# Kernel optimization log

Hardware: AMD Instinct MI355X
Metric: run time of the kernel (lower is better)

## Reference

```python
import jax, jax.numpy as jnp
import numpy as np

N, LP, LD, D, H, GS = 16, 2048, 512, 256, 8, 4
HD = D // H           # head_size = 32
TAU = 1.0             # softmax_tau
ITERS = 4             # sinkhorn_iters
INF = 1.0e6


def setup_inputs() -> dict:
    key = jax.random.key(0)
    ks = jax.random.split(key, 10)
    inp = {
        "protein": jax.random.normal(ks[0], (N, LP, D), jnp.float32),
        "drug": jax.random.normal(ks[1], (N, LD, D), jnp.float32),
        "mask_prot": jax.random.bernoulli(ks[2], 0.9, (N, LP)),
        "mask_drug": jax.random.bernoulli(ks[3], 0.9, (N, LD)),
    }
    names = ["Wq_p", "Wk_p", "Wv_p", "Wq_d", "Wk_d", "Wv_d"]
    for i, name in enumerate(names):
        inp[name] = jax.random.normal(ks[4 + i], (D, D), jnp.float32) * (1.0 / np.sqrt(D))
    return inp


def _group(x, mask):
    n, L, d = x.shape
    g = L // GS
    xg = x.reshape(n, g, GS, d).mean(2)          # [N,G,D]
    mg = mask.reshape(n, g, GS).any(2)           # [N,G]
    return xg, mg


def _alpha_logits(logits, mask_row, mask_col):
    # logits: [N,L1,L2,H]; sinkhorn normalization as in the torch module
    n, L1, L2, h = logits.shape
    logits = logits * (1.0 / np.sqrt(HD))
    pair = mask_row[:, :, None, None] & mask_col[:, None, :, None]  # [N,L1,L2,1]
    logits = jnp.where(pair, logits, logits - INF)
    A = jax.nn.softmax((logits / TAU).reshape(n, L1 * L2, h), axis=1).reshape(n, L1, L2, h)
    valid = pair.astype(A.dtype)
    A = A * valid + 1e-12 * valid
    for _ in range(ITERS):
        row_sum = (A * valid).sum(2, keepdims=True) + 1e-12
        A = A / row_sum * valid
        col_sum = (A * valid).sum(1, keepdims=True) + 1e-12
        A = A / col_sum * valid
    return A * valid


def _proj(x, W):
    n, g, d = x.shape
    return (x @ W.T).reshape(n, g, H, HD)


def reference(protein, drug, mask_prot, mask_drug, Wq_p, Wk_p, Wv_p, Wq_d, Wk_d, Wv_d):
    pg, mp = _group(protein, mask_prot)   # [N,Gp,D], [N,Gp]
    dg, md = _group(drug, mask_drug)      # [N,Gd,D], [N,Gd]

    qp, kp, vp = _proj(pg, Wq_p), _proj(pg, Wk_p), _proj(pg, Wv_p)
    qd, kd, vd = _proj(dg, Wq_d), _proj(dg, Wk_d), _proj(dg, Wv_d)

    att = lambda q, k: jnp.einsum('blhd,bkhd->blkh', q, k)
    a_pp = _alpha_logits(att(qp, kp), mp, mp)
    a_pd = _alpha_logits(att(qp, kd), mp, md)
    a_dp = _alpha_logits(att(qd, kp), md, mp)
    a_dd = _alpha_logits(att(qd, kd), md, md)

    mix = lambda a, v: jnp.einsum('blkh,bkhd->blhd', a, v).reshape(a.shape[0], a.shape[1], D)
    prot_embedding = (mix(a_pp, vp) + mix(a_pd, vd)) * 0.5  # [N,Gp,D]
    drug_embedding = (mix(a_dp, vp) + mix(a_dd, vd)) * 0.5  # [N,Gd,D]

    # agg_mode == 'mean': masked mean over valid groups
    mpf = mp[..., None].astype(prot_embedding.dtype)
    mdf = md[..., None].astype(drug_embedding.dtype)
    prot_embed = (prot_embedding * mpf).sum(1) / mpf.sum(1)
    drug_embed = (drug_embedding * mdf).sum(1) / mdf.sum(1)

    query_embed = jnp.concatenate([prot_embed, drug_embed], axis=1)  # [N,2D]
    return query_embed, a_dp
```

## Files before the change

kernel.cpp:

```cpp
#include <hip/hip_runtime.h>
#include <hip/hip_bf16.h>

#define NB   16
#define DT   256
#define HT   8
#define HDT  32
#define GP   512
#define GD   128

using bf16x8 = __attribute__((ext_vector_type(8))) short;
using f32x4  = __attribute__((ext_vector_type(4))) float;

__device__ __forceinline__ short f2bf(float f) {
  __hip_bfloat16 h = __float2bfloat16(f);
  short s; __builtin_memcpy(&s, &h, 2);
  return s;
}

extern "C" __global__ void k_prep(const float* __restrict__ Wk,
                                  const float* __restrict__ Wq,
                                  short* __restrict__ Wk_bf, short* __restrict__ Wq_bf,
                                  float* __restrict__ sp, float* __restrict__ sd,
                                  int* __restrict__ cnt) {
  int gid = blockIdx.x * 256 + threadIdx.x;
  if (gid < 65536) Wk_bf[gid] = f2bf(Wk[gid]);
  else             Wq_bf[gid - 65536] = f2bf(Wq[gid - 65536]);
  if (gid < 4096) sp[gid] = 0.f;
  else if (gid < 8192) sd[gid - 4096] = 0.f;
  if (gid < 32) cnt[gid] = 0;
}

extern "C" __global__ __launch_bounds__(256)
void k_group(const float* __restrict__ protein, const float* __restrict__ drug,
             const int* __restrict__ mprot, const int* __restrict__ mdrug,
             short* __restrict__ pg_bf, short* __restrict__ dg_bf,
             int* __restrict__ mp_g, int* __restrict__ md_g,
             float* __restrict__ sp, float* __restrict__ sd,
             int* __restrict__ cnt) {
  int b = blockIdx.x;
  int t = threadIdx.x;
  int n, c0, G;
  const float* src; const int* msk; short* dst; float* ssum; int* mg; int* cdst;
  if (b < 256) { n = b >> 4; c0 = (b & 15) * 32; G = GP;
                 src = protein; msk = mprot; dst = pg_bf; ssum = sp; mg = mp_g;
                 cdst = cnt + n; }
  else { int bb = b - 256; n = bb >> 2; c0 = (bb & 3) * 32; G = GD;
         src = drug; msk = mdrug; dst = dg_bf; ssum = sd; mg = md_g;
         cdst = cnt + 16 + n; }

  __shared__ int gmask[32];
  if (t < 32) {
    const int* m = msk + ((size_t)n * G + c0 + t) * 4;
    int v = (m[0] | m[1] | m[2] | m[3]) ? 1 : 0;
    gmask[t] = v;
    mg[n * G + c0 + t] = v;
  }
  __syncthreads();
  if (t == 0) {
    int c = 0;
    #pragma unroll
    for (int i = 0; i < 32; ++i) c += gmask[i];
    atomicAdd(cdst, c);
  }

  float acc_s = 0.f;
  const float* bp = src + ((size_t)n * G + c0) * 1024 + t;
  #pragma unroll 4
  for (int gi = 0; gi < 32; ++gi) {
    const float* rp = bp + (size_t)gi * 1024;
    float gm = 0.25f * (rp[0] + rp[256] + rp[512] + rp[768]);
    dst[((size_t)n * G + c0 + gi) * 256 + t] = f2bf(gm);
    if (gmask[gi]) acc_s += gm;
  }
  atomicAdd(&ssum[n * 256 + t], acc_s);
}

extern "C" __global__ __launch_bounds__(256)
void k_projbf(const short* __restrict__ pg_bf, const short* __restrict__ dg_bf,
              const short* __restrict__ Wk_bf, const short* __restrict__ Wq_bf,
              short* __restrict__ kp_bf, short* __restrict__ qd_bf) {
  int b = blockIdx.x;
  int w = threadIdx.x >> 6, lane = threadIdx.x & 63;
  int c15 = lane & 15, g = lane >> 4;
  const short *A, *W; short* out; int rt;
  if (b < 128) { A = pg_bf; W = Wk_bf; out = kp_bf; rt = b * 4 + w; }
  else         { A = dg_bf; W = Wq_bf; out = qd_bf; rt = (b - 128) * 4 + w; }

  const short* ap = A + ((size_t)rt * 16 + c15) * 256;
  f32x4 acc[16];
  #pragma unroll
  for (int i = 0; i < 16; ++i) acc[i] = (f32x4){0.f, 0.f, 0.f, 0.f};

  #pragma unroll
  for (int ks = 0; ks < 8; ++ks) {
    bf16x8 af = *(const bf16x8*)(ap + ks * 32 + g * 8);
    #pragma unroll
    for (int ct = 0; ct < 16; ++ct) {
      bf16x8 bfr = *(const bf16x8*)(W + ((size_t)(ct * 16 + c15)) * 256 + ks * 32 + g * 8);
      acc[ct] = __builtin_amdgcn_mfma_f32_16x16x32_bf16(af, bfr, acc[ct], 0, 0, 0);
    }
  }
  #pragma unroll
  for (int ct = 0; ct < 16; ++ct) {
    #pragma unroll
    for (int r = 0; r < 4; ++r) {
      out[((size_t)rt * 16 + 4 * g + r) * 256 + ct * 16 + c15] = f2bf(acc[ct][r]);
    }
  }
}

extern "C" __global__ __launch_bounds__(256)
void k_embed(const float* __restrict__ sp, const float* __restrict__ sd,
             const float* __restrict__ Wvp, const float* __restrict__ Wvd,
             const int* __restrict__ cnt, float* __restrict__ out) {
  int n = blockIdx.x >> 3;
  int dchunk = (blockIdx.x & 7) * 32;
  int t = threadIdx.x;
  __shared__ float sps[256], sds[256];
  sps[t] = sp[n * 256 + t];
  sds[t] = sd[n * 256 + t];
  __syncthreads();
  int dloc = t >> 3, ks = (t & 7) * 32;
  int d = dchunk + dloc;
  const float* wp = Wvp + (size_t)d * 256 + ks;
  const float* wd = Wvd + (size_t)d * 256 + ks;
  float acc = 0.f;
  #pragma unroll
  for (int k = 0; k < 32; k += 4) {
    float4 a = *(const float4*)(wp + k);
    float4 c = *(const float4*)(wd + k);
    acc += sps[ks + k] * a.x + sps[ks + k + 1] * a.y + sps[ks + k + 2] * a.z + sps[ks + k + 3] * a.w
         + sds[ks + k] * c.x + sds[ks + k + 1] * c.y + sds[ks + k + 2] * c.z + sds[ks + k + 3] * c.w;
  }
  #pragma unroll
  for (int m = 1; m <= 4; m <<= 1) acc += __shfl_xor(acc, m, 64);
  if ((t & 7) == 0) {
    acc *= 0.5f;
    out[n * 512 + d]       = acc / (float)cnt[n];
    out[n * 512 + 256 + d] = acc / (float)cnt[16 + n];
  }
}

extern "C" __global__ __launch_bounds__(512, 2)
void k_scalars(const short* __restrict__ qd, const short* __restrict__ kp,
               const int* __restrict__ md_g, const int* __restrict__ mp_g,
               float* __restrict__ rcz) {
  int bid = blockIdx.x;
  int n = ((bid & 7) << 1) | ((bid >> 3) & 1);
  int h = bid >> 4;
  int tid = threadIdx.x;
  int w = tid >> 6, lane = tid & 63;
  int c15 = lane & 15, g = lane >> 4;

  __shared__ float c_s[GP];
  __shared__ float r_s[GD];
  __shared__ float t_s[GD];
  __shared__ float red[8][GP];
  __shared__ float z_sh, sr_sh, sc_sh, kv_sh;
  __shared__ int mp_sh[GP];
  __shared__ int md_sh[GD];

  if (tid < GP) { int m = mp_g[n * GP + tid]; mp_sh[tid] = m; c_s[tid] = m ? 1.f : 0.f; }
  if (tid < GD) { int m = md_g[n * GD + tid]; md_sh[tid] = m; r_s[tid] = m ? 1.f : 0.f; }
  if (tid == 0) z_sh = 0.f;
  __syncthreads();

  if (w == 0) {
    float v = (float)(mp_sh[lane] + mp_sh[lane + 64] + mp_sh[lane + 128] + mp_sh[lane + 192] +
                      mp_sh[lane + 256] + mp_sh[lane + 320] + mp_sh[lane + 384] + mp_sh[lane + 448]);
    #pragma unroll
    for (int m = 1; m <= 32; m <<= 1) v += __shfl_xor(v, m, 64);
    if (lane == 0) kv_sh = v;
  }

  int qrow = 16 * w + c15;
  bf16x8 af = *(const bf16x8*)(qd + ((size_t)(n * GD + qrow)) * 256 + h * HDT + g * 8);

  float p[32][4];
  #pragma unroll
  for (int ct = 0; ct < 32; ++ct) {
    int krow = 16 * ct + c15;
    bf16x8 bfr = *(const bf16x8*)(kp + ((size_t)(n * GP + krow)) * 256 + h * HDT + g * 8);
    f32x4 acc = __builtin_amdgcn_mfma_f32_16x16x32_bf16(af, bfr, (f32x4){0.f,0.f,0.f,0.f}, 0, 0, 0);
    int mcol = mp_sh[16 * ct + c15];
    #pragma unroll
    for (int r = 0; r < 4; ++r) {
      int row = 16 * w + 4 * g + r;
      p[ct][r] = (mcol && md_sh[row]) ? __expf(acc[r] * 0.17677669529663687f) : 0.f;
    }
  }

  {
    float pa0 = 0.f, pa1 = 0.f, pa2 = 0.f, pa3 = 0.f;
    #pragma unroll
    for (int ct = 0; ct < 32; ++ct) {
      pa0 += p[ct][0]; pa1 += p[ct][1]; pa2 += p[ct][2]; pa3 += p[ct][3];
    }
    #pragma unroll
    for (int m = 1; m <= 8; m <<= 1) {
      pa0 += __shfl_xor(pa0, m, 64); pa1 += __shfl_xor(pa1, m, 64);
      pa2 += __shfl_xor(pa2, m, 64); pa3 += __shfl_xor(pa3, m, 64);
    }
    if (c15 == 0) t_s[16 * w + 4 * g + 0] = pa0;
    if (c15 == 1) t_s[16 * w + 4 * g + 1] = pa1;
    if (c15 == 2) t_s[16 * w + 4 * g + 2] = pa2;
    if (c15 == 3) t_s[16 * w + 4 * g + 3] = pa3;
  }
  __syncthreads();
  if (tid < GD) atomicAdd(&z_sh, t_s[tid]);
  __syncthreads();
  float Zinv = 1.0f / z_sh;
  float Sc = kv_sh;

  #pragma unroll 1
  for (int it = 0; it < 4; ++it) {
    if (tid < GD) {
      float ti = t_s[tid] * Zinv + 1e-12f * Sc;
      float ri = r_s[tid];
      r_s[tid] = md_sh[tid] ? (ri / (ri * ti + 1e-12f)) : 0.f;
    }
    __syncthreads();
    if (w == 0) {
      float v = r_s[lane] + r_s[lane + 64];
      #pragma unroll
      for (int m = 1; m <= 32; m <<= 1) v += __shfl_xor(v, m, 64);
      if (lane == 0) sr_sh = v;
    }
    __syncthreads();
    float Sr = sr_sh;
    float rr0 = r_s[16 * w + 4 * g + 0];
    float rr1 = r_s[16 * w + 4 * g + 1];
    float rr2 = r_s[16 * w + 4 * g + 2];
    float rr3 = r_s[16 * w + 4 * g + 3];
    #pragma unroll
    for (int ct = 0; ct < 32; ++ct) {
      float u = p[ct][0] * rr0 + p[ct][1] * rr1 + p[ct][2] * rr2 + p[ct][3] * rr3;
      u += __shfl_xor(u, 16, 64);
      u += __shfl_xor(u, 32, 64);
      if (g == 0) red[w][16 * ct + c15] = u;
    }
    __syncthreads();
    {
      float cs = red[0][tid] + red[1][tid] + red[2][tid] + red[3][tid] +
                 red[4][tid] + red[5][tid] + red[6][tid] + red[7][tid];
      float uj = cs * Zinv + 1e-12f * Sr;
      float cj = c_s[tid];
      c_s[tid] = mp_sh[tid] ? (cj / (cj * uj + 1e-12f)) : 0.f;
    }
    __syncthreads();
    if (w == 0) {
      float v = c_s[lane] + c_s[lane + 64] + c_s[lane + 128] + c_s[lane + 192] +
                c_s[lane + 256] + c_s[lane + 320] + c_s[lane + 384] + c_s[lane + 448];
      #pragma unroll
      for (int m = 1; m <= 32; m <<= 1) v += __shfl_xor(v, m, 64);
      if (lane == 0) sc_sh = v;
    }
    __syncthreads();
    Sc = sc_sh;
    if (it < 3) {
      float pa0 = 0.f, pa1 = 0.f, pa2 = 0.f, pa3 = 0.f;
      #pragma unroll
      for (int ct = 0; ct < 32; ++ct) {
        float cv = c_s[16 * ct + c15];
        pa0 += p[ct][0] * cv; pa1 += p[ct][1] * cv;
        pa2 += p[ct][2] * cv; pa3 += p[ct][3] * cv;
      }
      #pragma unroll
      for (int m = 1; m <= 8; m <<= 1) {
        pa0 += __shfl_xor(pa0, m, 64); pa1 += __shfl_xor(pa1, m, 64);
        pa2 += __shfl_xor(pa2, m, 64); pa3 += __shfl_xor(pa3, m, 64);
      }
      if (c15 == 0) t_s[16 * w + 4 * g + 0] = pa0;
      if (c15 == 1) t_s[16 * w + 4 * g + 1] = pa1;
      if (c15 == 2) t_s[16 * w + 4 * g + 2] = pa2;
      if (c15 == 3) t_s[16 * w + 4 * g + 3] = pa3;
      __syncthreads();
    }
  }

  size_t rb = (size_t)(n * 8 + h) * 1024;
  if (tid < GD) rcz[rb + tid] = r_s[tid];
  if (tid < GP) rcz[rb + 128 + tid] = c_s[tid];
  if (tid == 0) rcz[rb + 640] = Zinv;
}

extern "C" __global__ __launch_bounds__(256)
void k_write(const short* __restrict__ qd, const short* __restrict__ kp,
             const float* __restrict__ rcz, float* __restrict__ out) {
  int bid = blockIdx.x;
  int n = ((bid & 7) << 1) | ((bid >> 3) & 1);
  int rest = bid >> 4;
  int rt = rest >> 2;
  int cc = rest & 3;
  int w = threadIdx.x >> 6, lane = threadIdx.x & 63;
  int c15 = lane & 15, g = lane >> 4;

  const short* qbase = qd + ((size_t)(n * GD + rt * 16 + c15)) * 256;
  bf16x8 af[8];
  #pragma unroll
  for (int h = 0; h < 8; ++h) af[h] = *(const bf16x8*)(qbase + h * HDT + g * 8);

  size_t rb = (size_t)n * 8 * 1024;
  float rv[8][4], zin[8];
  #pragma unroll
  for (int h = 0; h < 8; ++h) {
    const float* rp = rcz + rb + (size_t)h * 1024;
    #pragma unroll
    for (int r = 0; r < 4; ++r) rv[h][r] = rp[rt * 16 + 4 * g + r];
    zin[h] = rp[640];
  }

  #pragma unroll
  for (int ct = 0; ct < 2; ++ct) {
    int col = cc * 128 + w * 32 + ct * 16 + c15;
    f32x4 acc[8]; float cw[8];
    #pragma unroll
    for (int h = 0; h < 8; ++h) {
      bf16x8 bfr = *(const bf16x8*)(kp + ((size_t)(n * GP + col)) * 256 + h * HDT + g * 8);
      acc[h] = __builtin_amdgcn_mfma_f32_16x16x32_bf16(af[h], bfr, (f32x4){0.f,0.f,0.f,0.f}, 0, 0, 0);
      cw[h] = rcz[rb + (size_t)h * 1024 + 128 + col];
    }
    #pragma unroll
    for (int r = 0; r < 4; ++r) {
      int row = rt * 16 + 4 * g + r;
      float4 lo, hi;
      lo.x = rv[0][r] * (__expf(acc[0][r] * 0.17677669529663687f) * zin[0] + 1e-12f) * cw[0];
      lo.y = rv[1][r] * (__expf(acc[1][r] * 0.17677669529663687f) * zin[1] + 1e-12f) * cw[1];
      lo.z = rv[2][r] * (__expf(acc[2][r] * 0.17677669529663687f) * zin[2] + 1e-12f) * cw[2];
      lo.w = rv[3][r] * (__expf(acc[3][r] * 0.17677669529663687f) * zin[3] + 1e-12f) * cw[3];
      hi.x = rv[4][r] * (__expf(acc[4][r] * 0.17677669529663687f) * zin[4] + 1e-12f) * cw[4];
      hi.y = rv[5][r] * (__expf(acc[5][r] * 0.17677669529663687f) * zin[5] + 1e-12f) * cw[5];
      hi.z = rv[6][r] * (__expf(acc[6][r] * 0.17677669529663687f) * zin[6] + 1e-12f) * cw[6];
      hi.w = rv[7][r] * (__expf(acc[7][r] * 0.17677669529663687f) * zin[7] + 1e-12f) * cw[7];
      float* dst = out + 8192 + (((size_t)(n * GD + row)) * GP + col) * 8;
      *(float4*)dst = lo;
      *(float4*)(dst + 4) = hi;
    }
  }
}

extern "C" void kernel_launch(void* const* d_in, const int* in_sizes, int n_in,
                              void* d_out, int out_size, void* d_ws, size_t ws_size,
                              hipStream_t stream) {
  const float* protein = (const float*)d_in[0];
  const float* drug    = (const float*)d_in[1];
  const int*   mprot   = (const int*)d_in[2];
  const int*   mdrug   = (const int*)d_in[3];
  const float* Wk_p = (const float*)d_in[5];
  const float* Wv_p = (const float*)d_in[6];
  const float* Wq_d = (const float*)d_in[7];
  const float* Wv_d = (const float*)d_in[9];
  float* out = (float*)d_out;

  char* wsb = (char*)d_ws;
  short* pg_bf = (short*)wsb;                 wsb += (size_t)NB * GP * 256 * 2;
  short* dg_bf = (short*)wsb;                 wsb += (size_t)NB * GD * 256 * 2;
  short* kp_bf = (short*)wsb;                 wsb += (size_t)NB * GP * 256 * 2;
  short* qd_bf = (short*)wsb;                 wsb += (size_t)NB * GD * 256 * 2;
  short* Wk_bf = (short*)wsb;                 wsb += 65536 * 2;
  short* Wq_bf = (short*)wsb;                 wsb += 65536 * 2;
  float* sp    = (float*)wsb;                 wsb += 4096 * 4;
  float* sd    = (float*)wsb;                 wsb += 4096 * 4;
  float* rcz   = (float*)wsb;                 wsb += (size_t)128 * 1024 * 4;
  int*   cnt   = (int*)wsb;                   wsb += 32 * 4;
  int*   mp_g  = (int*)wsb;                   wsb += 8192 * 4;
  int*   md_g  = (int*)wsb;                   wsb += 2048 * 4;

  k_prep<<<512, 256, 0, stream>>>(Wk_p, Wq_d, Wk_bf, Wq_bf, sp, sd, cnt);
  k_group<<<320, 256, 0, stream>>>(protein, drug, mprot, mdrug,
                                   pg_bf, dg_bf, mp_g, md_g, sp, sd, cnt);
  k_projbf<<<160, 256, 0, stream>>>(pg_bf, dg_bf, Wk_bf, Wq_bf, kp_bf, qd_bf);
  k_embed<<<128, 256, 0, stream>>>(sp, sd, Wv_p, Wv_d, cnt, out);
  k_scalars<<<128, 512, 0, stream>>>(qd_bf, kp_bf, md_g, mp_g, rcz);
  k_write<<<512, 256, 0, stream>>>(qd_bf, kp_bf, rcz, out);
}
```

Before: 194.3 us.

## Merge prep/group and proj/embed kernels, drop atomics, store scalars probabilities in fp16

Folds the weight-to-bf16 conversion into extra blocks of the grouping kernel, and the embedding matvec into extra blocks of the projection kernel. This cuts the launch count from six to four. Global atomics and their zero-init are replaced by per-block partial sums and counts, which the embed blocks reduce. In k_scalars the 32x4 probability register array becomes fp16 to lower register pressure, launch_bounds drops the min-blocks hint, and the Z reduction uses shuffles instead of shared atomics. The fp16 storage adds rounding error to the Sinkhorn scalars.

```diff
diff --git a/kernel.cpp b/kernel.cpp
--- a/kernel.cpp
+++ b/kernel.cpp
@@ -17,36 +17,32 @@
   return s;
 }
 
-extern "C" __global__ void k_prep(const float* __restrict__ Wk,
-                                  const float* __restrict__ Wq,
-                                  short* __restrict__ Wk_bf, short* __restrict__ Wq_bf,
-                                  float* __restrict__ sp, float* __restrict__ sd,
-                                  int* __restrict__ cnt) {
-  int gid = blockIdx.x * 256 + threadIdx.x;
-  if (gid < 65536) Wk_bf[gid] = f2bf(Wk[gid]);
-  else             Wq_bf[gid - 65536] = f2bf(Wq[gid - 65536]);
-  if (gid < 4096) sp[gid] = 0.f;
-  else if (gid < 8192) sd[gid - 4096] = 0.f;
-  if (gid < 32) cnt[gid] = 0;
-}
-
 extern "C" __global__ __launch_bounds__(256)
 void k_group(const float* __restrict__ protein, const float* __restrict__ drug,
              const int* __restrict__ mprot, const int* __restrict__ mdrug,
+             const float* __restrict__ Wk, const float* __restrict__ Wq,
              short* __restrict__ pg_bf, short* __restrict__ dg_bf,
              int* __restrict__ mp_g, int* __restrict__ md_g,
-             float* __restrict__ sp, float* __restrict__ sd,
-             int* __restrict__ cnt) {
+             short* __restrict__ Wk_bf, short* __restrict__ Wq_bf,
+             float* __restrict__ part, int* __restrict__ cntp) {
   int b = blockIdx.x;
   int t = threadIdx.x;
+  if (b >= 320) {
+    int base = (b - 320) * 512;
+    #pragma unroll
+    for (int j = 0; j < 2; ++j) {
+      int gid = base + t + j * 256;
+      if (gid < 65536) Wk_bf[gid] = f2bf(Wk[gid]);
+      else             Wq_bf[gid - 65536] = f2bf(Wq[gid - 65536]);
+    }
+    return;
+  }
   int n, c0, G;
-  const float* src; const int* msk; short* dst; float* ssum; int* mg; int* cdst;
+  const float* src; const int* msk; short* dst; int* mg;
   if (b < 256) { n = b >> 4; c0 = (b & 15) * 32; G = GP;
-                 src = protein; msk = mprot; dst = pg_bf; ssum = sp; mg = mp_g;
-                 cdst = cnt + n; }
+                 src = protein; msk = mprot; dst = pg_bf; mg = mp_g; }
   else { int bb = b - 256; n = bb >> 2; c0 = (bb & 3) * 32; G = GD;
-         src = drug; msk = mdrug; dst = dg_bf; ssum = sd; mg = md_g;
-         cdst = cnt + 16 + n; }
+         src = drug; msk = mdrug; dst = dg_bf; mg = md_g; }
 
   __shared__ int gmask[32];
   if (t < 32) {
@@ -60,7 +56,7 @@
     int c = 0;
     #pragma unroll
     for (int i = 0; i < 32; ++i) c += gmask[i];
-    atomicAdd(cdst, c);
+    cntp[b] = c;
   }
 
   float acc_s = 0.f;
@@ -72,19 +68,63 @@
     dst[((size_t)n * G + c0 + gi) * 256 + t] = f2bf(gm);
     if (gmask[gi]) acc_s += gm;
   }
-  atomicAdd(&ssum[n * 256 + t], acc_s);
+  part[(size_t)b * 256 + t] = acc_s;
 }
 
 extern "C" __global__ __launch_bounds__(256)
-void k_projbf(const short* __restrict__ pg_bf, const short* __restrict__ dg_bf,
-              const short* __restrict__ Wk_bf, const short* __restrict__ Wq_bf,
-              short* __restrict__ kp_bf, short* __restrict__ qd_bf) {
+void k_proj_embed(const short* __restrict__ pg_bf, const short* __restrict__ dg_bf,
+                  const short* __restrict__ Wk_bf, const short* __restrict__ Wq_bf,
+                  short* __restrict__ kp_bf, short* __restrict__ qd_bf,
+                  const float* __restrict__ part, const int* __restrict__ cntp,
+                  const float* __restrict__ Wvp, const float* __restrict__ Wvd,
+                  float* __restrict__ out) {
   int b = blockIdx.x;
-  int w = threadIdx.x >> 6, lane = threadIdx.x & 63;
+  int t = threadIdx.x;
+  if (b >= 160) {
+    int bb = b - 160;
+    int n = bb >> 3;
+    int dchunk = (bb & 7) * 32;
+    __shared__ float sps[256], sds[256];
+    float a1 = 0.f;
+    #pragma unroll
+    for (int i = 0; i < 16; ++i) a1 += part[(size_t)(n * 16 + i) * 256 + t];
+    sps[t] = a1;
+    float a2 = 0.f;
+    #pragma unroll
+    for (int i = 0; i < 4; ++i) a2 += part[(size_t)(256 + n * 4 + i) * 256 + t];
+    sds[t] = a2;
+    __syncthreads();
+    int cp = 0, cd = 0;
+    #pragma unroll
+    for (int i = 0; i < 16; ++i) cp += cntp[n * 16 + i];
+    #pragma unroll
+    for (int i = 0; i < 4; ++i) cd += cntp[256 + n * 4 + i];
+    int dloc = t >> 3, ks = (t & 7) * 32;
+    int d = dchunk + dloc;
+    const float* wp = Wvp + (size_t)d * 256 + ks;
+    const float* wd = Wvd + (size_t)d * 256 + ks;
+    float acc = 0.f;
+    #pragma unroll
+    for (int k = 0; k < 32; k += 4) {
+      float4 a = *(const float4*)(wp + k);
+      float4 c = *(const float4*)(wd + k);
+      acc += sps[ks + k] * a.x + sps[ks + k + 1] * a.y + sps[ks + k + 2] * a.z + sps[ks + k + 3] * a.w
+           + sds[ks + k] * c.x + sds[ks + k + 1] * c.y + sds[ks + k + 2] * c.z + sds[ks + k + 3] * c.w;
+    }
+    #pragma unroll
+    for (int m = 1; m <= 4; m <<= 1) acc += __shfl_xor(acc, m, 64);
+    if ((t & 7) == 0) {
+      acc *= 0.5f;
+      out[n * 512 + d]       = acc / (float)cp;
+      out[n * 512 + 256 + d] = acc / (float)cd;
+    }
+    return;
+  }
+  int w = t >> 6, lane = t & 63;
   int c15 = lane & 15, g = lane >> 4;
-  const short *A, *W; short* out; int rt;
-  if (b < 128) { A = pg_bf; W = Wk_bf; out = kp_bf; rt = b * 4 + w; }
-  else         { A = dg_bf; W = Wq_bf; out = qd_bf; rt = (b - 128) * 4 + w; }
+  const short *A, *W; short* o; int rt;
+  if (b < 128) { A = pg_bf; W = Wk_bf; o = kp_bf; rt = b * 4 + w; }
+  else         { A = dg_bf; W = Wq_bf; o = qd_bf; rt = (b - 128) * 4 + w; }
 
   const short* ap = A + ((size_t)rt * 16 + c15) * 256;
   f32x4 acc[16];
@@ -104,44 +144,12 @@
   for (int ct = 0; ct < 16; ++ct) {
     #pragma unroll
     for (int r = 0; r < 4; ++r) {
-      out[((size_t)rt * 16 + 4 * g + r) * 256 + ct * 16 + c15] = f2bf(acc[ct][r]);
-    }
-  }
-}
-
-extern "C" __global__ __launch_bounds__(256)
-void k_embed(const float* __restrict__ sp, const float* __restrict__ sd,
-             const float* __restrict__ Wvp, const float* __restrict__ Wvd,
-             const int* __restrict__ cnt, float* __restrict__ out) {
-  int n = blockIdx.x >> 3;
-  int dchunk = (blockIdx.x & 7) * 32;
-  int t = threadIdx.x;
-  __shared__ float sps[256], sds[256];
-  sps[t] = sp[n * 256 + t];
-  sds[t] = sd[n * 256 + t];
-  __syncthreads();
-  int dloc = t >> 3, ks = (t & 7) * 32;
-  int d = dchunk + dloc;
-  const float* wp = Wvp + (size_t)d * 256 + ks;
-  const float* wd = Wvd + (size_t)d * 256 + ks;
-  float acc = 0.f;
-  #pragma unroll
-  for (int k = 0; k < 32; k += 4) {
-    float4 a = *(const float4*)(wp + k);
-    float4 c = *(const float4*)(wd + k);
-    acc += sps[ks + k] * a.x + sps[ks + k + 1] * a.y + sps[ks + k + 2] * a.z + sps[ks + k + 3] * a.w
-         + sds[ks + k] * c.x + sds[ks + k + 1] * c.y + sds[ks + k + 2] * c.z + sds[ks + k + 3] * c.w;
-  }
-  #pragma unroll
-  for (int m = 1; m <= 4; m <<= 1) acc += __shfl_xor(acc, m, 64);
-  if ((t & 7) == 0) {
-    acc *= 0.5f;
-    out[n * 512 + d]       = acc / (float)cnt[n];
-    out[n * 512 + 256 + d] = acc / (float)cnt[16 + n];
-  }
-}
-
-extern "C" __global__ __launch_bounds__(512, 2)
+      o[((size_t)rt * 16 + 4 * g + r) * 256 + ct * 16 + c15] = f2bf(acc[ct][r]);
+    }
+  }
+}
+
+extern "C" __global__ __launch_bounds__(512)
 void k_scalars(const short* __restrict__ qd, const short* __restrict__ kp,
                const int* __restrict__ md_g, const int* __restrict__ mp_g,
                float* __restrict__ rcz) {
@@ -162,7 +170,6 @@
 
   if (tid < GP) { int m = mp_g[n * GP + tid]; mp_sh[tid] = m; c_s[tid] = m ? 1.f : 0.f; }
   if (tid < GD) { int m = md_g[n * GD + tid]; md_sh[tid] = m; r_s[tid] = m ? 1.f : 0.f; }
-  if (tid == 0) z_sh = 0.f;
   __syncthreads();
 
   if (w == 0) {
@@ -176,7 +183,7 @@
   int qrow = 16 * w + c15;
   bf16x8 af = *(const bf16x8*)(qd + ((size_t)(n * GD + qrow)) * 256 + h * HDT + g * 8);
 
-  float p[32][4];
+  _Float16 p[32][4];
   #pragma unroll
   for (int ct = 0; ct < 32; ++ct) {
     int krow = 16 * ct + c15;
@@ -186,7 +193,7 @@
     #pragma unroll
     for (int r = 0; r < 4; ++r) {
       int row = 16 * w + 4 * g + r;
-      p[ct][r] = (mcol && md_sh[row]) ? __expf(acc[r] * 0.17677669529663687f) : 0.f;
+      p[ct][r] = (_Float16)((mcol && md_sh[row]) ? __expf(acc[r] * 0.17677669529663687f) : 0.f);
     }
   }
 
@@ -194,7 +201,8 @@
     float pa0 = 0.f, pa1 = 0.f, pa2 = 0.f, pa3 = 0.f;
     #pragma unroll
     for (int ct = 0; ct < 32; ++ct) {
-      pa0 += p[ct][0]; pa1 += p[ct][1]; pa2 += p[ct][2]; pa3 += p[ct][3];
+      pa0 += (float)p[ct][0]; pa1 += (float)p[ct][1];
+      pa2 += (float)p[ct][2]; pa3 += (float)p[ct][3];
     }
     #pragma unroll
     for (int m = 1; m <= 8; m <<= 1) {
@@ -207,7 +215,12 @@
     if (c15 == 3) t_s[16 * w + 4 * g + 3] = pa3;
   }
   __syncthreads();
-  if (tid < GD) atomicAdd(&z_sh, t_s[tid]);
+  if (w == 0) {
+    float v = t_s[lane] + t_s[lane + 64];
+    #pragma unroll
+    for (int m = 1; m <= 32; m <<= 1) v += __shfl_xor(v, m, 64);
+    if (lane == 0) z_sh = v;
+  }
   __syncthreads();
   float Zinv = 1.0f / z_sh;
   float Sc = kv_sh;
@@ -234,7 +247,8 @@
     float rr3 = r_s[16 * w + 4 * g + 3];
     #pragma unroll
     for (int ct = 0; ct < 32; ++ct) {
-      float u = p[ct][0] * rr0 + p[ct][1] * rr1 + p[ct][2] * rr2 + p[ct][3] * rr3;
+      float u = (float)p[ct][0] * rr0 + (float)p[ct][1] * rr1 +
+                (float)p[ct][2] * rr2 + (float)p[ct][3] * rr3;
       u += __shfl_xor(u, 16, 64);
       u += __shfl_xor(u, 32, 64);
       if (g == 0) red[w][16 * ct + c15] = u;
@@ -262,8 +276,8 @@
       #pragma unroll
       for (int ct = 0; ct < 32; ++ct) {
         float cv = c_s[16 * ct + c15];
-        pa0 += p[ct][0] * cv; pa1 += p[ct][1] * cv;
-        pa2 += p[ct][2] * cv; pa3 += p[ct][3] * cv;
+        pa0 += (float)p[ct][0] * cv; pa1 += (float)p[ct][1] * cv;
+        pa2 += (float)p[ct][2] * cv; pa3 += (float)p[ct][3] * cv;
       }
       #pragma unroll
       for (int m = 1; m <= 8; m <<= 1) {
@@ -359,18 +373,17 @@
   short* qd_bf = (short*)wsb;                 wsb += (size_t)NB * GD * 256 * 2;
   short* Wk_bf = (short*)wsb;                 wsb += 65536 * 2;
   short* Wq_bf = (short*)wsb;                 wsb += 65536 * 2;
-  float* sp    = (float*)wsb;                 wsb += 4096 * 4;
-  float* sd    = (float*)wsb;                 wsb += 4096 * 4;
+  float* part  = (float*)wsb;                 wsb += (size_t)320 * 256 * 4;
   float* rcz   = (float*)wsb;                 wsb += (size_t)128 * 1024 * 4;
-  int*   cnt   = (int*)wsb;                   wsb += 32 * 4;
+  int*   cntp  = (int*)wsb;                   wsb += 320 * 4;
   int*   mp_g  = (int*)wsb;                   wsb += 8192 * 4;
   int*   md_g  = (int*)wsb;                   wsb += 2048 * 4;
 
-  k_prep<<<512, 256, 0, stream>>>(Wk_p, Wq_d, Wk_bf, Wq_bf, sp, sd, cnt);
-  k_group<<<320, 256, 0, stream>>>(protein, drug, mprot, mdrug,
-                                   pg_bf, dg_bf, mp_g, md_g, sp, sd, cnt);
-  k_projbf<<<160, 256, 0, stream>>>(pg_bf, dg_bf, Wk_bf, Wq_bf, kp_bf, qd_bf);
-  k_embed<<<128, 256, 0, stream>>>(sp, sd, Wv_p, Wv_d, cnt, out);
+  k_group<<<576, 256, 0, stream>>>(protein, drug, mprot, mdrug, Wk_p, Wq_d,
+                                   pg_bf, dg_bf, mp_g, md_g, Wk_bf, Wq_bf,
+                                   part, cntp);
+  k_proj_embed<<<288, 256, 0, stream>>>(pg_bf, dg_bf, Wk_bf, Wq_bf, kp_bf, qd_bf,
+                                        part, cntp, Wv_p, Wv_d, out);
   k_scalars<<<128, 512, 0, stream>>>(qd_bf, kp_bf, md_g, mp_g, rcz);
   k_write<<<512, 256, 0, stream>>>(qd_bf, kp_bf, rcz, out);
 }
```

Result: faster. 186.8 us (-3.9%).
